# Kernel optimization log

Hardware: AMD Instinct MI355X
Metric: run time of the kernel (lower is better)

The kernel has to match this reference:

```python
import jax, jax.numpy as jnp
import numpy as np

N_NODES = 100000
N_EDGES = 3200000
N_SG = 800000  # edges in the softmax-normalized segment
RULES = 9

SUB_MAT = np.array([[-0.2, -0.1, -0.05, -0.05, -0.05, -0.01, -0.055, -0.01, 0.0],
                    [0.0, -0.002, -0.001, -0.001, -0.001, -0.0002, 0.0008, -0.0002, 0.0]], dtype=np.float32)
SUB_BIAS = np.array([1, 0.7, 0.275, 0.4, 0.25, 0.07, 0.2225, 0.07, 0], dtype=np.float32)


def setup_inputs() -> dict:
    key = jax.random.key(0)
    k1, k2, k3 = jax.random.split(key, 3)
    feat = jax.random.normal(k1, (N_NODES, 4), dtype=jnp.float32)
    src = jax.random.randint(k2, (N_EDGES,), 0, N_NODES)
    dst = jax.random.randint(k3, (N_EDGES,), 0, N_NODES)
    edge_sg_ID = jnp.arange(N_SG, dtype=jnp.int64 if jax.config.read('jax_enable_x64') else jnp.int32).reshape(1, N_SG)
    return {
        'feat': feat,
        'src': src,
        'dst': dst,
        'edge_sg_ID': edge_sg_ID,
        'sub_systems_mat': jnp.asarray(SUB_MAT),
        'sub_systems_bias': jnp.asarray(SUB_BIAS),
    }


def _gauss(x, mean, sigma):
    return jnp.exp(-(x - mean) ** 2 / (2.0 * sigma ** 2))


def _ante_generator(vector):
    # vector: [E, 4] = (dpos_x, dpos_y, dvel_x, dvel_y)
    d = vector[:, :2]
    v = vector[:, 2:]
    x1 = jnp.linalg.norm(d, axis=1, keepdims=True)  # distance, [E,1]
    vnorm = jnp.linalg.norm(v, axis=1, keepdims=True)
    cos = jnp.sum(d * v, axis=1, keepdims=True) / (x1 * vnorm + 1e-8)
    x2 = jnp.degrees(jnp.arccos(jnp.clip(cos, -1.0 + 1e-6, 1.0 - 1e-6)))  # angle deg, [E,1]
    return x1, x2


def _ante_process(x1, x2):
    # memberships: x1 small/med/large, x2 small/med/large
    m1 = [_gauss(x1, 0.0, 0.75), _gauss(x1, 2.0, 0.75), _gauss(x1, 4.0, 0.75)]
    m2 = [_gauss(x2, 0.0, 30.0), _gauss(x2, 90.0, 30.0), _gauss(x2, 180.0, 30.0)]
    # 9 rules: min over all (x1_level, x2_level) pairs -> [E, 1, 9]
    return jnp.stack([jnp.minimum(a, b) for a in m1 for b in m2], axis=2)


def _forward(feat, sub_systems_mat, sub_systems_bias, src, dst, edge_sg_ID):
    vector = feat[dst] - feat[src]  # [E, 4]
    x1, x2 = _ante_generator(vector)  # each [E, 1]
    truth = _ante_process(x1, x2)  # [E, 1, 9]
    premises = jnp.stack((x1, x2), axis=2).reshape(-1, 2)  # [E, 2]
    consequence = premises @ sub_systems_mat + sub_systems_bias  # [E, 9]
    consequence = consequence.reshape(x1.shape[0], x1.shape[1], RULES)  # [E, 1, 9]
    attention = jnp.sum(truth * consequence, axis=2) / jnp.sum(truth, axis=2)  # [E, 1]
    attention = attention[:, :, None]  # [E, 1, 1]
    idx = edge_sg_ID[0]
    # segment softmax over the selected edges (dim 0)
    attention = attention.at[idx].set(jax.nn.softmax(attention[idx], axis=0))
    return attention


def reference(feat, src, dst, edge_sg_ID, sub_systems_mat, sub_systems_bias):
    return _forward(feat, sub_systems_mat, sub_systems_bias, src, dst, edge_sg_ID)
```

## Files before the change

kernel.cpp:

```cpp
#include <hip/hip_runtime.h>

#define N_NODES 100000
#define N_EDGES 3200000
#define N_SG    800000
#define RULES   9
#define BLOCK   256

#define K1_BLOCKS    1536
#define K1_THREADS   (K1_BLOCKS * BLOCK)
#define MAIN_GROUPS  (K1_THREADS * 2)
#define TOT_GROUPS   (N_EDGES / 4)
#define REM_GROUPS   (TOT_GROUPS - MAIN_GROUPS)
#define REM_PER_BLK  9
#define SG_GROUPS    (N_SG / 4)
#define SOFT_THREADS (N_SG / 8)
#define K2_BLOCKS    768

typedef float vf4 __attribute__((ext_vector_type(4)));
typedef int   vi4 __attribute__((ext_vector_type(4)));


__device__ __forceinline__ float fast_acos_deg(float x)
{
    float ax = fabsf(x);
    float p = fmaf(ax, -0.0187293f, 0.0742610f);
    p = fmaf(p, ax, -0.2121144f);
    p = fmaf(p, ax, 1.5707288f);
    float r = __builtin_amdgcn_sqrtf(1.0f - ax) * p;
    r = (x < 0.0f) ? (3.14159265358979f - r) : r;
    return r * 57.29577951308232f;
}

__device__ __forceinline__ float edge_attn(vf4 fd, vf4 fs,
                                           const float* c1, const float* c2,
                                           const float* cb)
{
    float d0 = fd.x - fs.x, d1 = fd.y - fs.y;
    float v0 = fd.z - fs.z, v1 = fd.w - fs.w;

    float d2  = fmaf(d0, d0, d1 * d1);
    float v2  = fmaf(v0, v0, v1 * v1);
    float x1  = __builtin_amdgcn_sqrtf(d2);
    float dot = fmaf(d0, v0, d1 * v1);
    float cosv = dot * __builtin_amdgcn_rcpf(
                     __builtin_amdgcn_sqrtf(d2 * v2) + 1e-8f);
    cosv = fminf(fmaxf(cosv, -1.0f + 1e-6f), 1.0f - 1e-6f);
    float x2 = fast_acos_deg(cosv);

    const float k1 = 0.888888888888889f;
    const float k2 = 5.555555555555556e-4f;
    float m1[3], m2[3];
    float a;
    a = x1;          m1[0] = __expf(-a * a * k1);
    a = x1 - 2.0f;   m1[1] = __expf(-a * a * k1);
    a = x1 - 4.0f;   m1[2] = __expf(-a * a * k1);
    a = x2;          m2[0] = __expf(-a * a * k2);
    a = x2 - 90.0f;  m2[1] = __expf(-a * a * k2);
    a = x2 - 180.0f; m2[2] = __expf(-a * a * k2);

    float num = 0.0f, den = 0.0f;
#pragma unroll
    for (int i = 0; i < 3; ++i) {
#pragma unroll
        for (int j = 0; j < 3; ++j) {
            int r = i * 3 + j;
            float t = fminf(m1[i], m2[j]);
            float c = fmaf(x1, c1[r], fmaf(x2, c2[r], cb[r]));
            num = fmaf(t, c, num);
            den += t;
        }
    }
    return num * __builtin_amdgcn_rcpf(den);
}

__global__ __launch_bounds__(BLOCK, 4) void edge_attn_kernel(
    const vf4*  __restrict__ feat,
    const vi4*  __restrict__ src4,
    const vi4*  __restrict__ dst4,
    const float* __restrict__ M,
    const float* __restrict__ B,
    vf4*        __restrict__ out4,
    float*      __restrict__ partials)
{
    const int T = blockIdx.x * BLOCK + threadIdx.x;

    float c1[RULES], c2[RULES], cb[RULES];
#pragma unroll
    for (int r = 0; r < RULES; ++r) {
        c1[r] = M[r];
        c2[r] = M[RULES + r];
        cb[r] = B[r];
    }

    vi4 sa = __builtin_nontemporal_load(&src4[2 * T]);
    vi4 sb = __builtin_nontemporal_load(&src4[2 * T + 1]);
    vi4 da = __builtin_nontemporal_load(&dst4[2 * T]);
    vi4 db = __builtin_nontemporal_load(&dst4[2 * T + 1]);

    vf4 fs0 = feat[sa.x], fs1 = feat[sa.y], fs2 = feat[sa.z], fs3 = feat[sa.w];
    vf4 fs4 = feat[sb.x], fs5 = feat[sb.y], fs6 = feat[sb.z], fs7 = feat[sb.w];
    vf4 fd0 = feat[da.x], fd1 = feat[da.y], fd2 = feat[da.z], fd3 = feat[da.w];
    vf4 fd4 = feat[db.x], fd5 = feat[db.y], fd6 = feat[db.z], fd7 = feat[db.w];

    vf4 ra, rb;
    ra.x = edge_attn(fd0, fs0, c1, c2, cb);
    ra.y = edge_attn(fd1, fs1, c1, c2, cb);
    ra.z = edge_attn(fd2, fs2, c1, c2, cb);
    ra.w = edge_attn(fd3, fs3, c1, c2, cb);
    rb.x = edge_attn(fd4, fs4, c1, c2, cb);
    rb.y = edge_attn(fd5, fs5, c1, c2, cb);
    rb.z = edge_attn(fd6, fs6, c1, c2, cb);
    rb.w = edge_attn(fd7, fs7, c1, c2, cb);

    float s = 0.0f;
    if (T < SOFT_THREADS) {
        ra.x = __expf(ra.x); ra.y = __expf(ra.y);
        ra.z = __expf(ra.z); ra.w = __expf(ra.w);
        rb.x = __expf(rb.x); rb.y = __expf(rb.y);
        rb.z = __expf(rb.z); rb.w = __expf(rb.w);
        s = (ra.x + ra.y + ra.z + ra.w) + (rb.x + rb.y + rb.z + rb.w);
        out4[2 * T]     = ra;
        out4[2 * T + 1] = rb;
    } else {
        __builtin_nontemporal_store(ra, &out4[2 * T]);
        __builtin_nontemporal_store(rb, &out4[2 * T + 1]);
    }

    if (threadIdx.x < REM_PER_BLK) {
        int e = blockIdx.x * REM_PER_BLK + threadIdx.x;
        if (e < REM_GROUPS) {
            int g = MAIN_GROUPS + e;
            vi4 sr = __builtin_nontemporal_load(&src4[g]);
            vi4 dr = __builtin_nontemporal_load(&dst4[g]);
            vf4 gs0 = feat[sr.x], gs1 = feat[sr.y], gs2 = feat[sr.z], gs3 = feat[sr.w];
            vf4 gd0 = feat[dr.x], gd1 = feat[dr.y], gd2 = feat[dr.z], gd3 = feat[dr.w];
            vf4 rr;
            rr.x = edge_attn(gd0, gs0, c1, c2, cb);
            rr.y = edge_attn(gd1, gs1, c1, c2, cb);
            rr.z = edge_attn(gd2, gs2, c1, c2, cb);
            rr.w = edge_attn(gd3, gs3, c1, c2, cb);
            __builtin_nontemporal_store(rr, &out4[g]);
        }
    }

#pragma unroll
    for (int o = 32; o > 0; o >>= 1) s += __shfl_down(s, o, 64);
    __shared__ float wsum[BLOCK / 64];
    if ((threadIdx.x & 63) == 0) wsum[threadIdx.x >> 6] = s;
    __syncthreads();
    if (threadIdx.x == 0)
        partials[blockIdx.x] = wsum[0] + wsum[1] + wsum[2] + wsum[3];
}

__global__ __launch_bounds__(BLOCK) void softmax_write_kernel(
    const float* __restrict__ partials,
    vf4*         __restrict__ out4)
{
    float s = 0.0f;
#pragma unroll
    for (int p = threadIdx.x; p < K1_BLOCKS; p += BLOCK) s += partials[p];
#pragma unroll
    for (int o = 32; o > 0; o >>= 1) s += __shfl_down(s, o, 64);
    __shared__ float wsum[BLOCK / 64];
    if ((threadIdx.x & 63) == 0) wsum[threadIdx.x >> 6] = s;
    __syncthreads();
    float inv = 1.0f / (wsum[0] + wsum[1] + wsum[2] + wsum[3]);

    for (int i = blockIdx.x * BLOCK + threadIdx.x; i < SG_GROUPS;
         i += K2_BLOCKS * BLOCK) {
        vf4 v = out4[i];
        v.x *= inv; v.y *= inv; v.z *= inv; v.w *= inv;
        out4[i] = v;
    }
}

extern "C" void kernel_launch(void* const* d_in, const int* in_sizes, int n_in,
                              void* d_out, int out_size, void* d_ws, size_t ws_size,
                              hipStream_t stream)
{
    const vf4*   feat = (const vf4*)d_in[0];
    const vi4*   src4 = (const vi4*)d_in[1];
    const vi4*   dst4 = (const vi4*)d_in[2];
    const float* M    = (const float*)d_in[4];
    const float* B    = (const float*)d_in[5];
    vf4*   out4     = (vf4*)d_out;
    float* partials = (float*)d_ws;

    edge_attn_kernel<<<dim3(K1_BLOCKS), dim3(BLOCK), 0, stream>>>(
        feat, src4, dst4, M, B, out4, partials);
    softmax_write_kernel<<<dim3(K2_BLOCKS), dim3(BLOCK), 0, stream>>>(
        partials, out4);
}
```

Before: 118.9 us.

## Fuse edge attention and softmax normalization via cooperative grid sync

Replaces the two-kernel scheme with a single cooperative kernel. Each thread handles three strided edge groups and keeps its softmax-segment exponentials in registers. After a grid-wide sync it reduces the per-block partial sums and writes the normalized values directly, avoiding a second launch and the re-read/re-write of the softmax segment. The grid shrinks to 1024 blocks, and a two-kernel fallback is kept for when the occupancy query reports fewer than four blocks per CU. The cost is a grid.sync barrier, an occupancy query on every launch, and more register pressure from holding the values across the barrier.

New measurement: 116.9 us. About the same (-1.6%).

```diff
diff --git a/kernel.cpp b/kernel.cpp
--- a/kernel.cpp
+++ b/kernel.cpp
@@ -1,20 +1,19 @@
 #include <hip/hip_runtime.h>
-
-#define N_NODES 100000
+#include <hip/hip_cooperative_groups.h>
+
+namespace cg = cooperative_groups;
+
 #define N_EDGES 3200000
 #define N_SG    800000
 #define RULES   9
 #define BLOCK   256
-
-#define K1_BLOCKS    1536
-#define K1_THREADS   (K1_BLOCKS * BLOCK)
-#define MAIN_GROUPS  (K1_THREADS * 2)
-#define TOT_GROUPS   (N_EDGES / 4)
-#define REM_GROUPS   (TOT_GROUPS - MAIN_GROUPS)
-#define REM_PER_BLK  9
-#define SG_GROUPS    (N_SG / 4)
-#define SOFT_THREADS (N_SG / 8)
-#define K2_BLOCKS    768
+#define GRID    1024
+#define NT      (GRID * BLOCK)
+#define TOT_GROUPS (N_EDGES / 4)
+#define SG_GROUPS  (N_SG / 4)
+#define FULL3      (3 * NT)
+#define TAILN      (TOT_GROUPS - FULL3)
+#define TAIL_PER_BLK 14
 
 typedef float vf4 __attribute__((ext_vector_type(4)));
 typedef int   vi4 __attribute__((ext_vector_type(4)));
@@ -73,16 +72,31 @@
     return num * __builtin_amdgcn_rcpf(den);
 }
 
-__global__ __launch_bounds__(BLOCK, 4) void edge_attn_kernel(
-    const vf4*  __restrict__ feat,
-    const vi4*  __restrict__ src4,
-    const vi4*  __restrict__ dst4,
+__device__ __forceinline__ vf4 attn_group(vi4 s, vi4 d, const vf4* feat,
+                                          const float* c1, const float* c2,
+                                          const float* cb)
+{
+    vf4 a0 = feat[s.x], a1 = feat[s.y], a2 = feat[s.z], a3 = feat[s.w];
+    vf4 b0 = feat[d.x], b1 = feat[d.y], b2 = feat[d.z], b3 = feat[d.w];
+    vf4 r;
+    r.x = edge_attn(b0, a0, c1, c2, cb);
+    r.y = edge_attn(b1, a1, c1, c2, cb);
+    r.z = edge_attn(b2, a2, c1, c2, cb);
+    r.w = edge_attn(b3, a3, c1, c2, cb);
+    return r;
+}
+
+__global__ __launch_bounds__(BLOCK, 4) void fused_kernel(
+    const vf4*   __restrict__ feat,
+    const vi4*   __restrict__ src4,
+    const vi4*   __restrict__ dst4,
     const float* __restrict__ M,
     const float* __restrict__ B,
-    vf4*        __restrict__ out4,
-    float*      __restrict__ partials)
-{
-    const int T = blockIdx.x * BLOCK + threadIdx.x;
+    vf4*         __restrict__ out4,
+    float*       __restrict__ partials)
+{
+    cg::grid_group grid = cg::this_grid();
+    const int t = blockIdx.x * BLOCK + threadIdx.x;
 
     float c1[RULES], c2[RULES], cb[RULES];
 #pragma unroll
@@ -92,57 +106,118 @@
         cb[r] = B[r];
     }
 
-    vi4 sa = __builtin_nontemporal_load(&src4[2 * T]);
-    vi4 sb = __builtin_nontemporal_load(&src4[2 * T + 1]);
-    vi4 da = __builtin_nontemporal_load(&dst4[2 * T]);
-    vi4 db = __builtin_nontemporal_load(&dst4[2 * T + 1]);
-
-    vf4 fs0 = feat[sa.x], fs1 = feat[sa.y], fs2 = feat[sa.z], fs3 = feat[sa.w];
-    vf4 fs4 = feat[sb.x], fs5 = feat[sb.y], fs6 = feat[sb.z], fs7 = feat[sb.w];
-    vf4 fd0 = feat[da.x], fd1 = feat[da.y], fd2 = feat[da.z], fd3 = feat[da.w];
-    vf4 fd4 = feat[db.x], fd5 = feat[db.y], fd6 = feat[db.z], fd7 = feat[db.w];
-
-    vf4 ra, rb;
-    ra.x = edge_attn(fd0, fs0, c1, c2, cb);
-    ra.y = edge_attn(fd1, fs1, c1, c2, cb);
-    ra.z = edge_attn(fd2, fs2, c1, c2, cb);
-    ra.w = edge_attn(fd3, fs3, c1, c2, cb);
-    rb.x = edge_attn(fd4, fs4, c1, c2, cb);
-    rb.y = edge_attn(fd5, fs5, c1, c2, cb);
-    rb.z = edge_attn(fd6, fs6, c1, c2, cb);
-    rb.w = edge_attn(fd7, fs7, c1, c2, cb);
+    const int g0 = t, g1 = t + NT, g2 = t + 2 * NT;
+    vi4 s0 = __builtin_nontemporal_load(&src4[g0]);
+    vi4 d0 = __builtin_nontemporal_load(&dst4[g0]);
+    vi4 s1 = __builtin_nontemporal_load(&src4[g1]);
+    vi4 d1 = __builtin_nontemporal_load(&dst4[g1]);
+    vi4 s2 = __builtin_nontemporal_load(&src4[g2]);
+    vi4 d2 = __builtin_nontemporal_load(&dst4[g2]);
+
+    vf4 a0 = feat[s0.x], a1 = feat[s0.y], a2 = feat[s0.z], a3 = feat[s0.w];
+    vf4 b0 = feat[d0.x], b1 = feat[d0.y], b2 = feat[d0.z], b3 = feat[d0.w];
+    vf4 e0 = feat[s1.x], e1 = feat[s1.y], e2 = feat[s1.z], e3 = feat[s1.w];
+    vf4 f0 = feat[d1.x], f1 = feat[d1.y], f2 = feat[d1.z], f3 = feat[d1.w];
+
+    vf4 ra;
+    ra.x = edge_attn(b0, a0, c1, c2, cb);
+    ra.y = edge_attn(b1, a1, c1, c2, cb);
+    ra.z = edge_attn(b2, a2, c1, c2, cb);
+    ra.w = edge_attn(b3, a3, c1, c2, cb);
 
     float s = 0.0f;
-    if (T < SOFT_THREADS) {
+    const bool soft = (t < SG_GROUPS);
+    if (soft) {
         ra.x = __expf(ra.x); ra.y = __expf(ra.y);
         ra.z = __expf(ra.z); ra.w = __expf(ra.w);
-        rb.x = __expf(rb.x); rb.y = __expf(rb.y);
-        rb.z = __expf(rb.z); rb.w = __expf(rb.w);
-        s = (ra.x + ra.y + ra.z + ra.w) + (rb.x + rb.y + rb.z + rb.w);
-        out4[2 * T]     = ra;
-        out4[2 * T + 1] = rb;
+        s = (ra.x + ra.y) + (ra.z + ra.w);
     } else {
-        __builtin_nontemporal_store(ra, &out4[2 * T]);
-        __builtin_nontemporal_store(rb, &out4[2 * T + 1]);
-    }
-
-    if (threadIdx.x < REM_PER_BLK) {
-        int e = blockIdx.x * REM_PER_BLK + threadIdx.x;
-        if (e < REM_GROUPS) {
-            int g = MAIN_GROUPS + e;
+        __builtin_nontemporal_store(ra, &out4[g0]);
+    }
+
+    vf4 rb;
+    rb.x = edge_attn(f0, e0, c1, c2, cb);
+    rb.y = edge_attn(f1, e1, c1, c2, cb);
+    rb.z = edge_attn(f2, e2, c1, c2, cb);
+    rb.w = edge_attn(f3, e3, c1, c2, cb);
+    __builtin_nontemporal_store(rb, &out4[g1]);
+
+    vf4 rc = attn_group(s2, d2, feat, c1, c2, cb);
+    __builtin_nontemporal_store(rc, &out4[g2]);
+
+    if (threadIdx.x < TAIL_PER_BLK) {
+        int e = blockIdx.x * TAIL_PER_BLK + threadIdx.x;
+        if (e < TAILN) {
+            int g = FULL3 + e;
             vi4 sr = __builtin_nontemporal_load(&src4[g]);
             vi4 dr = __builtin_nontemporal_load(&dst4[g]);
-            vf4 gs0 = feat[sr.x], gs1 = feat[sr.y], gs2 = feat[sr.z], gs3 = feat[sr.w];
-            vf4 gd0 = feat[dr.x], gd1 = feat[dr.y], gd2 = feat[dr.z], gd3 = feat[dr.w];
-            vf4 rr;
-            rr.x = edge_attn(gd0, gs0, c1, c2, cb);
-            rr.y = edge_attn(gd1, gs1, c1, c2, cb);
-            rr.z = edge_attn(gd2, gs2, c1, c2, cb);
-            rr.w = edge_attn(gd3, gs3, c1, c2, cb);
+            vf4 rr = attn_group(sr, dr, feat, c1, c2, cb);
             __builtin_nontemporal_store(rr, &out4[g]);
         }
     }
 
+    __shared__ float wsum[BLOCK / 64];
+    __shared__ float stot;
+#pragma unroll
+    for (int o = 32; o > 0; o >>= 1) s += __shfl_down(s, o, 64);
+    if ((threadIdx.x & 63) == 0) wsum[threadIdx.x >> 6] = s;
+    __syncthreads();
+    if (threadIdx.x == 0)
+        partials[blockIdx.x] = wsum[0] + wsum[1] + wsum[2] + wsum[3];
+
+    grid.sync();
+
+    float ts = partials[threadIdx.x]
+             + partials[threadIdx.x + 256]
+             + partials[threadIdx.x + 512]
+             + partials[threadIdx.x + 768];
+#pragma unroll
+    for (int o = 32; o > 0; o >>= 1) ts += __shfl_down(ts, o, 64);
+    if ((threadIdx.x & 63) == 0) wsum[threadIdx.x >> 6] = ts;
+    __syncthreads();
+    if (threadIdx.x == 0) stot = wsum[0] + wsum[1] + wsum[2] + wsum[3];
+    __syncthreads();
+
+    if (soft) {
+        float inv = 1.0f / stot;
+        ra.x *= inv; ra.y *= inv; ra.z *= inv; ra.w *= inv;
+        out4[g0] = ra;
+    }
+}
+
+#define FB_THREADS (N_EDGES / 8)
+#define FB_BLOCKS  ((FB_THREADS + BLOCK - 1) / BLOCK)
+#define FB_SOFT    (N_SG / 8)
+#define FB_K2_BLKS ((SG_GROUPS + BLOCK - 1) / BLOCK)
+
+__global__ __launch_bounds__(BLOCK, 4) void fb_edge_kernel(
+    const vf4* __restrict__ feat, const vi4* __restrict__ src4,
+    const vi4* __restrict__ dst4, const float* __restrict__ M,
+    const float* __restrict__ B, vf4* __restrict__ out4,
+    float* __restrict__ partials)
+{
+    int t = blockIdx.x * BLOCK + threadIdx.x;
+    float s = 0.0f;
+    float c1[RULES], c2[RULES], cb[RULES];
+#pragma unroll
+    for (int r = 0; r < RULES; ++r) {
+        c1[r] = M[r]; c2[r] = M[RULES + r]; cb[r] = B[r];
+    }
+    if (t < FB_THREADS) {
+        vi4 sa = src4[2 * t], sb = src4[2 * t + 1];
+        vi4 da = dst4[2 * t], db = dst4[2 * t + 1];
+        vf4 ra = attn_group(sa, da, feat, c1, c2, cb);
+        vf4 rb = attn_group(sb, db, feat, c1, c2, cb);
+        if (t < FB_SOFT) {
+            ra.x = __expf(ra.x); ra.y = __expf(ra.y);
+            ra.z = __expf(ra.z); ra.w = __expf(ra.w);
+            rb.x = __expf(rb.x); rb.y = __expf(rb.y);
+            rb.z = __expf(rb.z); rb.w = __expf(rb.w);
+            s = (ra.x + ra.y + ra.z + ra.w) + (rb.x + rb.y + rb.z + rb.w);
+        }
+        out4[2 * t] = ra;
+        out4[2 * t + 1] = rb;
+    }
 #pragma unroll
     for (int o = 32; o > 0; o >>= 1) s += __shfl_down(s, o, 64);
     __shared__ float wsum[BLOCK / 64];
@@ -152,22 +227,19 @@
         partials[blockIdx.x] = wsum[0] + wsum[1] + wsum[2] + wsum[3];
 }
 
-__global__ __launch_bounds__(BLOCK) void softmax_write_kernel(
-    const float* __restrict__ partials,
-    vf4*         __restrict__ out4)
+__global__ __launch_bounds__(BLOCK) void fb_softmax_kernel(
+    const float* __restrict__ partials, vf4* __restrict__ out4)
 {
     float s = 0.0f;
-#pragma unroll
-    for (int p = threadIdx.x; p < K1_BLOCKS; p += BLOCK) s += partials[p];
+    for (int p = threadIdx.x; p < FB_BLOCKS; p += BLOCK) s += partials[p];
 #pragma unroll
     for (int o = 32; o > 0; o >>= 1) s += __shfl_down(s, o, 64);
     __shared__ float wsum[BLOCK / 64];
     if ((threadIdx.x & 63) == 0) wsum[threadIdx.x >> 6] = s;
     __syncthreads();
     float inv = 1.0f / (wsum[0] + wsum[1] + wsum[2] + wsum[3]);
-
-    for (int i = blockIdx.x * BLOCK + threadIdx.x; i < SG_GROUPS;
-         i += K2_BLOCKS * BLOCK) {
+    int i = blockIdx.x * BLOCK + threadIdx.x;
+    if (i < SG_GROUPS) {
         vf4 v = out4[i];
         v.x *= inv; v.y *= inv; v.z *= inv; v.w *= inv;
         out4[i] = v;
@@ -186,8 +258,21 @@
     vf4*   out4     = (vf4*)d_out;
     float* partials = (float*)d_ws;
 
-    edge_attn_kernel<<<dim3(K1_BLOCKS), dim3(BLOCK), 0, stream>>>(
-        feat, src4, dst4, M, B, out4, partials);
-    softmax_write_kernel<<<dim3(K2_BLOCKS), dim3(BLOCK), 0, stream>>>(
-        partials, out4);
-}
+    int bpc = 0;
+    hipOccupancyMaxActiveBlocksPerMultiprocessor(&bpc,
+        (const void*)fused_kernel, BLOCK, 0);
+
+    if (bpc >= 4) {
+        void* args[] = {
+            (void*)&feat, (void*)&src4, (void*)&dst4,
+            (void*)&M, (void*)&B, (void*)&out4, (void*)&partials
+        };
+        hipLaunchCooperativeKernel((const void*)fused_kernel,
+                                   dim3(GRID), dim3(BLOCK), args, 0, stream);
+    } else {
+        fb_edge_kernel<<<dim3(FB_BLOCKS), dim3(BLOCK), 0, stream>>>(
+            feat, src4, dst4, M, B, out4, partials);
+        fb_softmax_kernel<<<dim3(FB_K2_BLKS), dim3(BLOCK), 0, stream>>>(
+            partials, out4);
+    }
+}
```

## Gather node features with inline-asm sc0 loads and launch one thread per 8 edges

Applied to the files above, without the earlier changes.

Replaces the compiler-generated feature gathers with inline-asm global_load_dwordx4 instructions carrying the sc0 cache-policy bit, issuing all 16 loads before a single wait. The edge kernel now launches one thread per 8-edge group instead of a fixed 1536-block grid with a remainder path, and drops the occupancy hint in launch_bounds. Nontemporal index loads and output stores become plain accesses. The softmax kernel's grid-stride loop becomes a full-coverage grid, and each of its blocks now reads more partial sums. The intent is better latency hiding and cache behaviour on the random gathers, at the cost of relying on hand-written asm and a larger grid.

Result: no change. 117.2 us (-1.4%).

```diff
diff --git a/kernel.cpp b/kernel.cpp
--- a/kernel.cpp
+++ b/kernel.cpp
@@ -6,15 +6,11 @@
 #define RULES   9
 #define BLOCK   256
 
-#define K1_BLOCKS    1536
-#define K1_THREADS   (K1_BLOCKS * BLOCK)
-#define MAIN_GROUPS  (K1_THREADS * 2)
-#define TOT_GROUPS   (N_EDGES / 4)
-#define REM_GROUPS   (TOT_GROUPS - MAIN_GROUPS)
-#define REM_PER_BLK  9
-#define SG_GROUPS    (N_SG / 4)
+#define K1_THREADS (N_EDGES / 8)
+#define K1_BLOCKS  ((K1_THREADS + BLOCK - 1) / BLOCK)
+#define SG_GROUPS  (N_SG / 4)
 #define SOFT_THREADS (N_SG / 8)
-#define K2_BLOCKS    768
+#define K2_BLOCKS  ((SG_GROUPS + BLOCK - 1) / BLOCK)
 
 typedef float vf4 __attribute__((ext_vector_type(4)));
 typedef int   vi4 __attribute__((ext_vector_type(4)));
@@ -73,74 +69,99 @@
     return num * __builtin_amdgcn_rcpf(den);
 }
 
-__global__ __launch_bounds__(BLOCK, 4) void edge_attn_kernel(
-    const vf4*  __restrict__ feat,
-    const vi4*  __restrict__ src4,
-    const vi4*  __restrict__ dst4,
+__device__ __forceinline__ void gather16_sc0(
+    const vf4* __restrict__ feat, vi4 sa, vi4 sb, vi4 da, vi4 db,
+    vf4& fs0, vf4& fs1, vf4& fs2, vf4& fs3,
+    vf4& fs4, vf4& fs5, vf4& fs6, vf4& fs7,
+    vf4& fd0, vf4& fd1, vf4& fd2, vf4& fd3,
+    vf4& fd4, vf4& fd5, vf4& fd6, vf4& fd7)
+{
+    const vf4 *p0 = feat + sa.x, *p1 = feat + sa.y, *p2 = feat + sa.z, *p3 = feat + sa.w;
+    const vf4 *p4 = feat + sb.x, *p5 = feat + sb.y, *p6 = feat + sb.z, *p7 = feat + sb.w;
+    const vf4 *q0 = feat + da.x, *q1 = feat + da.y, *q2 = feat + da.z, *q3 = feat + da.w;
+    const vf4 *q4 = feat + db.x, *q5 = feat + db.y, *q6 = feat + db.z, *q7 = feat + db.w;
+
+    asm volatile(
+        "global_load_dwordx4 %0, %8, off sc0\n\t"
+        "global_load_dwordx4 %1, %9, off sc0\n\t"
+        "global_load_dwordx4 %2, %10, off sc0\n\t"
+        "global_load_dwordx4 %3, %11, off sc0\n\t"
+        "global_load_dwordx4 %4, %12, off sc0\n\t"
+        "global_load_dwordx4 %5, %13, off sc0\n\t"
+        "global_load_dwordx4 %6, %14, off sc0\n\t"
+        "global_load_dwordx4 %7, %15, off sc0"
+        : "=&v"(fs0), "=&v"(fs1), "=&v"(fs2), "=&v"(fs3),
+          "=&v"(fs4), "=&v"(fs5), "=&v"(fs6), "=&v"(fs7)
+        : "v"(p0), "v"(p1), "v"(p2), "v"(p3),
+          "v"(p4), "v"(p5), "v"(p6), "v"(p7));
+
+    asm volatile(
+        "global_load_dwordx4 %0, %16, off sc0\n\t"
+        "global_load_dwordx4 %1, %17, off sc0\n\t"
+        "global_load_dwordx4 %2, %18, off sc0\n\t"
+        "global_load_dwordx4 %3, %19, off sc0\n\t"
+        "global_load_dwordx4 %4, %20, off sc0\n\t"
+        "global_load_dwordx4 %5, %21, off sc0\n\t"
+        "global_load_dwordx4 %6, %22, off sc0\n\t"
+        "global_load_dwordx4 %7, %23, off sc0\n\t"
+        "s_waitcnt vmcnt(0)"
+        : "=&v"(fd0), "=&v"(fd1), "=&v"(fd2), "=&v"(fd3),
+          "=&v"(fd4), "=&v"(fd5), "=&v"(fd6), "=&v"(fd7),
+          "+v"(fs0), "+v"(fs1), "+v"(fs2), "+v"(fs3),
+          "+v"(fs4), "+v"(fs5), "+v"(fs6), "+v"(fs7)
+        : "v"(q0), "v"(q1), "v"(q2), "v"(q3),
+          "v"(q4), "v"(q5), "v"(q6), "v"(q7));
+}
+
+__global__ __launch_bounds__(BLOCK) void edge_attn_kernel(
+    const vf4*   __restrict__ feat,
+    const vi4*   __restrict__ src4,
+    const vi4*   __restrict__ dst4,
     const float* __restrict__ M,
     const float* __restrict__ B,
-    vf4*        __restrict__ out4,
-    float*      __restrict__ partials)
-{
-    const int T = blockIdx.x * BLOCK + threadIdx.x;
-
-    float c1[RULES], c2[RULES], cb[RULES];
-#pragma unroll
-    for (int r = 0; r < RULES; ++r) {
-        c1[r] = M[r];
-        c2[r] = M[RULES + r];
-        cb[r] = B[r];
-    }
-
-    vi4 sa = __builtin_nontemporal_load(&src4[2 * T]);
-    vi4 sb = __builtin_nontemporal_load(&src4[2 * T + 1]);
-    vi4 da = __builtin_nontemporal_load(&dst4[2 * T]);
-    vi4 db = __builtin_nontemporal_load(&dst4[2 * T + 1]);
-
-    vf4 fs0 = feat[sa.x], fs1 = feat[sa.y], fs2 = feat[sa.z], fs3 = feat[sa.w];
-    vf4 fs4 = feat[sb.x], fs5 = feat[sb.y], fs6 = feat[sb.z], fs7 = feat[sb.w];
-    vf4 fd0 = feat[da.x], fd1 = feat[da.y], fd2 = feat[da.z], fd3 = feat[da.w];
-    vf4 fd4 = feat[db.x], fd5 = feat[db.y], fd6 = feat[db.z], fd7 = feat[db.w];
-
-    vf4 ra, rb;
-    ra.x = edge_attn(fd0, fs0, c1, c2, cb);
-    ra.y = edge_attn(fd1, fs1, c1, c2, cb);
-    ra.z = edge_attn(fd2, fs2, c1, c2, cb);
-    ra.w = edge_attn(fd3, fs3, c1, c2, cb);
-    rb.x = edge_attn(fd4, fs4, c1, c2, cb);
-    rb.y = edge_attn(fd5, fs5, c1, c2, cb);
-    rb.z = edge_attn(fd6, fs6, c1, c2, cb);
-    rb.w = edge_attn(fd7, fs7, c1, c2, cb);
-
+    vf4*         __restrict__ out4,
+    float*       __restrict__ partials)
+{
+    int t = blockIdx.x * BLOCK + threadIdx.x;
     float s = 0.0f;
-    if (T < SOFT_THREADS) {
-        ra.x = __expf(ra.x); ra.y = __expf(ra.y);
-        ra.z = __expf(ra.z); ra.w = __expf(ra.w);
-        rb.x = __expf(rb.x); rb.y = __expf(rb.y);
-        rb.z = __expf(rb.z); rb.w = __expf(rb.w);
-        s = (ra.x + ra.y + ra.z + ra.w) + (rb.x + rb.y + rb.z + rb.w);
-        out4[2 * T]     = ra;
-        out4[2 * T + 1] = rb;
-    } else {
-        __builtin_nontemporal_store(ra, &out4[2 * T]);
-        __builtin_nontemporal_store(rb, &out4[2 * T + 1]);
-    }
-
-    if (threadIdx.x < REM_PER_BLK) {
-        int e = blockIdx.x * REM_PER_BLK + threadIdx.x;
-        if (e < REM_GROUPS) {
-            int g = MAIN_GROUPS + e;
-            vi4 sr = __builtin_nontemporal_load(&src4[g]);
-            vi4 dr = __builtin_nontemporal_load(&dst4[g]);
-            vf4 gs0 = feat[sr.x], gs1 = feat[sr.y], gs2 = feat[sr.z], gs3 = feat[sr.w];
-            vf4 gd0 = feat[dr.x], gd1 = feat[dr.y], gd2 = feat[dr.z], gd3 = feat[dr.w];
-            vf4 rr;
-            rr.x = edge_attn(gd0, gs0, c1, c2, cb);
-            rr.y = edge_attn(gd1, gs1, c1, c2, cb);
-            rr.z = edge_attn(gd2, gs2, c1, c2, cb);
-            rr.w = edge_attn(gd3, gs3, c1, c2, cb);
-            __builtin_nontemporal_store(rr, &out4[g]);
+
+    if (t < K1_THREADS) {
+        vi4 sa = src4[2 * t], sb = src4[2 * t + 1];
+        vi4 da = dst4[2 * t], db = dst4[2 * t + 1];
+
+        vf4 fs0, fs1, fs2, fs3, fs4, fs5, fs6, fs7;
+        vf4 fd0, fd1, fd2, fd3, fd4, fd5, fd6, fd7;
+        gather16_sc0(feat, sa, sb, da, db,
+                     fs0, fs1, fs2, fs3, fs4, fs5, fs6, fs7,
+                     fd0, fd1, fd2, fd3, fd4, fd5, fd6, fd7);
+
+        float c1[RULES], c2[RULES], cb[RULES];
+#pragma unroll
+        for (int r = 0; r < RULES; ++r) {
+            c1[r] = M[r];
+            c2[r] = M[RULES + r];
+            cb[r] = B[r];
         }
+
+        vf4 ra, rb;
+        ra.x = edge_attn(fd0, fs0, c1, c2, cb);
+        ra.y = edge_attn(fd1, fs1, c1, c2, cb);
+        ra.z = edge_attn(fd2, fs2, c1, c2, cb);
+        ra.w = edge_attn(fd3, fs3, c1, c2, cb);
+        rb.x = edge_attn(fd4, fs4, c1, c2, cb);
+        rb.y = edge_attn(fd5, fs5, c1, c2, cb);
+        rb.z = edge_attn(fd6, fs6, c1, c2, cb);
+        rb.w = edge_attn(fd7, fs7, c1, c2, cb);
+
+        if (t < SOFT_THREADS) {
+            ra.x = __expf(ra.x); ra.y = __expf(ra.y);
+            ra.z = __expf(ra.z); ra.w = __expf(ra.w);
+            rb.x = __expf(rb.x); rb.y = __expf(rb.y);
+            rb.z = __expf(rb.z); rb.w = __expf(rb.w);
+            s = (ra.x + ra.y + ra.z + ra.w) + (rb.x + rb.y + rb.z + rb.w);
+        }
+        out4[2 * t]     = ra;
+        out4[2 * t + 1] = rb;
     }
 
 #pragma unroll
@@ -157,7 +178,6 @@
     vf4*         __restrict__ out4)
 {
     float s = 0.0f;
-#pragma unroll
     for (int p = threadIdx.x; p < K1_BLOCKS; p += BLOCK) s += partials[p];
 #pragma unroll
     for (int o = 32; o > 0; o >>= 1) s += __shfl_down(s, o, 64);
@@ -166,8 +186,8 @@
     __syncthreads();
     float inv = 1.0f / (wsum[0] + wsum[1] + wsum[2] + wsum[3]);
 
-    for (int i = blockIdx.x * BLOCK + threadIdx.x; i < SG_GROUPS;
-         i += K2_BLOCKS * BLOCK) {
+    int i = blockIdx.x * BLOCK + threadIdx.x;
+    if (i < SG_GROUPS) {
         vf4 v = out4[i];
         v.x *= inv; v.y *= inv; v.z *= inv; v.w *= inv;
         out4[i] = v;
```
